# Kernel optimization log

Measured on AMD Instinct MI355X. Metric: run time of the kernel, lower is better.

Reference implementation:

```python
import jax, jax.numpy as jnp
import numpy as np

# Config mirroring MultiHeadAttention1d(in_channels=256, n_heads=8, residual=False,
# kernel_size=1, attention_type=0) applied to 3-D inputs (B, C, N).
B, C, N, H, D = 4, 256, 2048, 8, 256  # per-head dim D = in_channels; OC = H*D = 2048
OC = H * D


def setup_inputs() -> dict:
    key = jax.random.key(0)
    ks = jax.random.split(key, 14)
    s = 1.0 / np.sqrt(C)
    f32 = jnp.float32
    inp = {
        "x": jax.random.normal(ks[0], (B, C, N), f32),
        "y": jax.random.normal(ks[1], (B, C, N), f32),
        # ConvNormActivation1d (kernel_size=1) == pointwise conv + (folded, eval-mode)
        # BatchNorm affine + ReLU. BN folds to per-channel scale g and shift beta.
        "Wq": jax.random.normal(ks[2], (OC, C), f32) * s,
        "bq": jax.random.normal(ks[3], (OC,), f32) * 0.01,
        "gq": jnp.ones((OC,), f32),
        "betaq": jnp.zeros((OC,), f32),
        "Wk": jax.random.normal(ks[4], (OC, C), f32) * s,
        "bk": jax.random.normal(ks[5], (OC,), f32) * 0.01,
        "gk": jnp.ones((OC,), f32),
        "betak": jnp.zeros((OC,), f32),
        "Wv": jax.random.normal(ks[6], (OC, C), f32) * s,
        "bv": jax.random.normal(ks[7], (OC,), f32) * 0.01,
        "gv": jnp.ones((OC,), f32),
        "betav": jnp.zeros((OC,), f32),
    }
    return inp


def _cna(W, b, g, beta, t):
    # 1x1 conv (channel GEMM) + folded-BN affine + ReLU; t: (B, C, N) -> (B, OC, N)
    z = jnp.einsum("oc,bcn->bon", W, t) + b[:, None]
    return jax.nn.relu(g[:, None] * z + beta[:, None])


def _heads(t):
    # (B, OC, N) -> (B, H, N, D); channel split matches torch.split chunks of size D
    return t.reshape(B, H, D, N).transpose(0, 1, 3, 2)


def reference(x, y, Wq, bq, gq, betaq, Wk, bk, gk, betak, Wv, bv, gv, betav):
    q = _heads(_cna(Wq, bq, gq, betaq, x))  # (B,H,N,D)
    k = _heads(_cna(Wk, bk, gk, betak, y))
    v = _heads(_cna(Wv, bv, gv, betav, y))
    energy = jnp.einsum("bhnd,bhmd->bhnm", q, k)  # bmm(Q, K^T)
    attn = jax.nn.softmax(energy, axis=-1)
    out = jnp.einsum("bhnm,bhmd->bhnd", attn, v)  # (B,H,N,D)
    # torch path: view(H,B,k,N,D).permute(1,0,3,2,4) -> (B,H,N,k=1,D);
    # squeeze(dim=2) is a no-op since N != 1.
    return out[:, :, :, None, :]  # (B, H, N, 1, D)
```

## Files before the change

### kernel.cpp

```cpp
#include <hip/hip_runtime.h>
#include <cstdint>
#include <cstddef>

typedef unsigned short u16;
typedef __attribute__((ext_vector_type(4))) float f32x4;
typedef __attribute__((ext_vector_type(16))) float f32x16;
typedef __attribute__((ext_vector_type(8))) _Float16 f16x8;
typedef __attribute__((ext_vector_type(4))) u16   u16x4;
typedef __attribute__((ext_vector_type(8))) u16   u16x8;
typedef __attribute__((ext_vector_type(4))) int   i32x4;

#define DEV static __device__ __forceinline__
#define MFMA16(a,b,c) __builtin_amdgcn_mfma_f32_16x16x32_f16((a),(b),(c),0,0,0)
#define MFMA32(a,b,c) __builtin_amdgcn_mfma_f32_32x32x16_f16((a),(b),(c),0,0,0)

constexpr int Bc = 4, Cc = 256, Nc = 2048, Hc = 8, Dc = 256, OCc = 2048;

constexpr size_t OFF_XT = 0;
constexpr size_t OFF_YT = OFF_XT + (size_t)Bc*Nc*Cc*2;
constexpr size_t OFF_WQ = OFF_YT + (size_t)Bc*Nc*Cc*2;
constexpr size_t OFF_WK = OFF_WQ + (size_t)OCc*Cc*2;
constexpr size_t OFF_WV = OFF_WK + (size_t)OCc*Cc*2;
constexpr size_t OFF_BQ = OFF_WV + (size_t)OCc*Cc*2;
constexpr size_t OFF_BK = OFF_BQ + (size_t)OCc*4;
constexpr size_t OFF_BV = OFF_BK + (size_t)OCc*4;
constexpr size_t OFF_Q  = OFF_BV + (size_t)OCc*4;
constexpr size_t OFF_K  = OFF_Q  + (size_t)Bc*Hc*Nc*Dc*2;
constexpr size_t OFF_V  = OFF_K  + (size_t)Bc*Hc*Nc*Dc*2;

DEV u16 f2h(float x){
  _Float16 h = (_Float16)x;
  return __builtin_bit_cast(u16, h);
}

DEV void load_lds16(const void* g, void* l){
  __builtin_amdgcn_global_load_lds((const __attribute__((address_space(1))) int*)g,
                                   (__attribute__((address_space(3))) int*)l, 16, 0, 0);
}

__global__ __launch_bounds__(256) void transpose_cast(const float* __restrict__ x,
                                                      const float* __restrict__ y,
                                                      u16* __restrict__ XT,
                                                      u16* __restrict__ YT){
  __shared__ u16 tile[64][65];
  int b = blockIdx.z >> 1;
  const float* src = (blockIdx.z & 1) ? y : x;
  u16* dst = (blockIdx.z & 1) ? YT : XT;
  int n0 = blockIdx.x * 64, c0 = blockIdx.y * 64;
  int t = threadIdx.x;
#pragma unroll
  for (int i = 0; i < 16; ++i){
    int slot = i*256 + t;
    int cl = slot >> 6, nl = slot & 63;
    tile[cl][nl] = f2h(src[((size_t)b*Cc + c0 + cl)*Nc + n0 + nl]);
  }
  __syncthreads();
#pragma unroll
  for (int i = 0; i < 8; ++i){
    int slot = i*256 + t;
    int nl = slot >> 5, cl = (slot & 31)*2;
    uint32_t v = (uint32_t)tile[cl][nl] | ((uint32_t)tile[cl+1][nl] << 16);
    *(uint32_t*)(dst + ((size_t)b*Nc + n0 + nl)*Cc + c0 + cl) = v;
  }
}

__global__ __launch_bounds__(256) void prep_w(const float* __restrict__ W,
                                              const float* __restrict__ bsrc,
                                              const float* __restrict__ g,
                                              const float* __restrict__ beta,
                                              u16* __restrict__ Wo,
                                              float* __restrict__ bb){
  int idx = (blockIdx.x*256 + threadIdx.x) * 8;
  int o = idx >> 8, c = idx & 255;
  float gg = g[o];
  f32x4 a0 = *(const f32x4*)(W + idx);
  f32x4 a1 = *(const f32x4*)(W + idx + 4);
  u16x8 r;
#pragma unroll
  for (int i = 0; i < 4; ++i){ r[i] = f2h(a0[i]*gg); r[i+4] = f2h(a1[i]*gg); }
  *(u16x8*)(Wo + idx) = r;
  if (c == 0) bb[o] = gg*bsrc[o] + beta[o];
}

template<int SW>
__global__ __launch_bounds__(256, 2) void proj_gemm(const u16* __restrict__ Xt,
                                                    const u16* __restrict__ Wp,
                                                    const float* __restrict__ bb,
                                                    u16* __restrict__ outp){
  __shared__ __align__(16) char lds[32768];
  int t = threadIdx.x, w = t >> 6, l = t & 63, q = l & 15, g = l >> 4;
  int b = blockIdx.z;
  int n0 = blockIdx.x * 128, o0 = blockIdx.y * 128;
  int fs = ((q >> 1) & 3) << 4;
  int partg = ((l & 3) ^ ((l >> 3) & 3));
  f32x4 acc[4][4] = {};

  for (int it = 0; it < 4; ++it){
    __syncthreads();
#pragma unroll
    for (int j = 0; j < 8; ++j){
      int s = j*4 + w;
      int chunk = s >> 3;
      int off = (s & 7) * 1024;
      int row = (s & 7)*16 + (l >> 2);
      const char* gsrc;
      if (chunk < 2)
        gsrc = (const char*)(Wp + (size_t)(o0 + row)*Cc) + it*128 + chunk*64 + partg*16;
      else
        gsrc = (const char*)(Xt + ((size_t)b*Nc + n0 + row)*Cc) + it*128 + (chunk & 1)*64 + partg*16;
      load_lds16(gsrc, lds + chunk*8192 + off);
    }
    asm volatile("s_waitcnt vmcnt(0)" ::: "memory");
    __syncthreads();
#pragma unroll
    for (int kc = 0; kc < 2; ++kc){
      f16x8 fw[4], fx[4];
#pragma unroll
      for (int i = 0; i < 4; ++i){
        int wrow = (SW ? (w & 1) : (w >> 1))*64 + i*16 + q;
        int xrow = (SW ? (w >> 1) : (w & 1))*64 + i*16 + q;
        fw[i] = *(const f16x8*)(lds + kc*8192 + wrow*64 + ((g*16) ^ fs));
        fx[i] = *(const f16x8*)(lds + 16384 + kc*8192 + xrow*64 + ((g*16) ^ fs));
      }
#pragma unroll
      for (int i = 0; i < 4; ++i)
#pragma unroll
        for (int jj = 0; jj < 4; ++jj){
          if constexpr (!SW) acc[i][jj] = MFMA16(fw[i], fx[jj], acc[i][jj]);
          else               acc[i][jj] = MFMA16(fx[i], fw[jj], acc[i][jj]);
        }
    }
  }

  if constexpr (!SW) {
    f32x4 bias[4];
#pragma unroll
    for (int i = 0; i < 4; ++i) bias[i] = *(const f32x4*)(bb + o0 + (w>>1)*64 + i*16 + 4*g);
#pragma unroll
    for (int i = 0; i < 4; ++i)
#pragma unroll
      for (int jj = 0; jj < 4; ++jj){
        u16x4 pk;
#pragma unroll
        for (int r = 0; r < 4; ++r){
          float z = acc[i][jj][r] + bias[i][r];
          pk[r] = f2h(fmaxf(z, 0.f));
        }
        int o = o0 + (w>>1)*64 + i*16 + 4*g;
        int n = n0 + (w&1)*64 + jj*16 + q;
        int hh = o >> 8, d = o & 255;
        *(u16x4*)(outp + ((size_t)((b*Hc + hh)*Nc + n))*Dc + d) = pk;
      }
  } else {
    float biasv[4];
#pragma unroll
    for (int i = 0; i < 4; ++i) biasv[i] = bb[o0 + (w&1)*64 + i*16 + q];
#pragma unroll
    for (int i = 0; i < 4; ++i)
#pragma unroll
      for (int jj = 0; jj < 4; ++jj){
        u16x4 pk;
#pragma unroll
        for (int r = 0; r < 4; ++r){
          float z = acc[i][jj][r] + biasv[jj];
          pk[r] = f2h(fmaxf(z, 0.f));
        }
        int o = o0 + (w&1)*64 + jj*16 + q;
        int n = n0 + (w>>1)*64 + i*16 + 4*g;
        int hh = o >> 8, d = o & 255;
        *(u16x4*)(outp + ((size_t)((b*Hc + hh)*Dc + d))*Nc + n) = pk;
      }
  }
}

__global__ __launch_bounds__(512, 1) void attn_kernel(const u16* __restrict__ Qp,
                                                      const u16* __restrict__ Kp,
                                                      const u16* __restrict__ Vp,
                                                      float* __restrict__ outp){
  __shared__ __align__(16) char lds[150528];
  const int t = threadIdx.x, w = t >> 6, l = t & 63, lq = l & 31, hi = l >> 5;
  const int wq = w & 3, wm = w >> 2;
  const int h = blockIdx.y, b = blockIdx.z;
  const int q0 = blockIdx.x * 128;
  size_t head = (size_t)(b*Hc + h) * Nc * Dc;
  const u16* Qh = Qp + head;
  const u16* Kh = Kp + head;
  const u16* Vh = Vp + head;

  char* Pex  = lds + 131072;
  float* smax = (float*)(lds + 147456);
  float* ssum = (float*)(lds + 148480);

  f16x8 qf[16];
  {
    const u16* qrow = Qh + (size_t)(q0 + wq*32 + lq) * Dc;
#pragma unroll
    for (int kc = 0; kc < 16; ++kc) qf[kc] = *(const f16x8*)(qrow + kc*16 + hi*8);
  }

  f32x16 acc[4] = {};
  float m_run = -1e30f, l_run = 0.f;
  const int lsw = lq ^ ((lq >> 3) & 3);

#define STAGE_KV(m0_, buf_)                                                        \
  {                                                                                \
    char* Kd = lds + (buf_)*32768;                                                 \
    char* Vd = lds + 65536 + (buf_)*32768;                                         \
    _Pragma("unroll")                                                              \
    for (int j = 0; j < 4; ++j){                                                   \
      int row = w*8 + j*2 + hi;                                                    \
      int r5 = row & 31;                                                           \
      int gs = (l & 31) ^ r5 ^ ((r5 >> 3) & 3);                                    \
      load_lds16(Kh + (size_t)((m0_) + row)*Dc + gs*8, Kd + w*4096 + j*1024);      \
    }                                                                              \
    _Pragma("unroll")                                                              \
    for (int j = 0; j < 4; ++j){                                                   \
      int ri = w*4 + j;                                                            \
      int rd = ri*8 + (l >> 3);                                                    \
      int gs = (l & 7) ^ (rd & 7);                                                 \
      load_lds16(Vh + (size_t)rd*Nc + (m0_) + gs*8, Vd + ri*1024);                 \
    }                                                                              \
  }

  STAGE_KV(0, 0);
  asm volatile("s_waitcnt vmcnt(0)" ::: "memory");
  __syncthreads();

  for (int it = 0; it < 32; ++it){
    const int cur = it & 1;
    char* Kc = lds + cur*32768;
    char* Vc = lds + 65536 + cur*32768;

    if (it < 31) STAGE_KV((it + 1)*64, cur ^ 1);

    f32x16 s = {};
    __builtin_amdgcn_s_setprio(1);
#pragma unroll
    for (int kc = 0; kc < 16; ++kc){
      f16x8 kf = *(const f16x8*)(Kc + (wm*32 + lq)*512 + (((kc*2 + hi) ^ lsw) << 4));
      s = MFMA32(kf, qf[kc], s);
    }
    __builtin_amdgcn_s_setprio(0);

    float tmax = s[0];
#pragma unroll
    for (int r = 1; r < 16; ++r) tmax = fmaxf(tmax, s[r]);
    tmax = fmaxf(tmax, __shfl_xor(tmax, 32));
    if (!hi) smax[(wq*2 + wm)*32 + lq] = tmax;
    __syncthreads();
    float omax = smax[(wq*2 + (1 - wm))*32 + lq];
    float cmax = fmaxf(tmax, omax);

    float meff = m_run, scale = 1.f;
    const bool need = !__all(cmax <= m_run + 8.f);
    if (need){
      meff = fmaxf(m_run, cmax);
      scale = __expf(m_run - meff);
      m_run = meff;
    }

    float p[16];
    float rsum = 0.f;
#pragma unroll
    for (int r = 0; r < 16; ++r){ p[r] = __expf(s[r] - meff); rsum += p[r]; }
    rsum += __shfl_xor(rsum, 32);
    if (!hi) ssum[(wq*2 + wm)*32 + lq] = rsum;

    int pk[8];
#pragma unroll
    for (int j2 = 0; j2 < 8; ++j2)
      pk[j2] = __builtin_bit_cast(int, __builtin_amdgcn_cvt_pkrtz(p[2*j2], p[2*j2+1]));
    int sx[8];
#pragma unroll
    for (int j2 = 0; j2 < 8; ++j2) sx[j2] = __shfl_xor(pk[j2], 32);
    i32x4 f0, f1;
    f0[0] = hi ? sx[2] : pk[0];  f0[1] = hi ? sx[3] : pk[1];
    f0[2] = hi ? pk[2] : sx[0];  f0[3] = hi ? pk[3] : sx[1];
    f1[0] = hi ? sx[6] : pk[4];  f1[1] = hi ? sx[7] : pk[5];
    f1[2] = hi ? pk[6] : sx[4];  f1[3] = hi ? pk[7] : sx[5];
    *(i32x4*)(Pex + w*2048 + l*16)        = f0;
    *(i32x4*)(Pex + w*2048 + 1024 + l*16) = f1;
    __syncthreads();

    float osum = ssum[(wq*2 + (1 - wm))*32 + lq];
    l_run = l_run * scale + rsum + osum;

    if (need){
#pragma unroll
      for (int r = 0; r < 16; ++r){
        float scr = __shfl(scale, (r & 3) + 8*(r >> 2) + 4*hi);
#pragma unroll
        for (int dt = 0; dt < 4; ++dt) acc[dt][r] *= scr;
      }
    }

    i32x4 g0 = *(const i32x4*)(Pex + (w ^ 4)*2048 + l*16);
    i32x4 g1 = *(const i32x4*)(Pex + (w ^ 4)*2048 + 1024 + l*16);
    f16x8 a0 = __builtin_bit_cast(f16x8, wm ? g0 : f0);
    f16x8 a1 = __builtin_bit_cast(f16x8, wm ? g1 : f1);
    f16x8 a2 = __builtin_bit_cast(f16x8, wm ? f0 : g0);
    f16x8 a3 = __builtin_bit_cast(f16x8, wm ? f1 : g1);

    __builtin_amdgcn_s_setprio(1);
#pragma unroll
    for (int h2 = 0; h2 < 2; ++h2)
#pragma unroll
      for (int dt = 0; dt < 4; ++dt)
#pragma unroll
        for (int mcl = 0; mcl < 2; ++mcl){
          f16x8 vf = *(const f16x8*)(Vc + (wm*128 + dt*32 + lq)*128 +
                                     (((h2*4 + mcl*2 + hi)*16) ^ ((l & 7) << 4)));
          f16x8 af = h2 ? (mcl ? a3 : a2) : (mcl ? a1 : a0);
          acc[dt] = MFMA32(af, vf, acc[dt]);
        }
    __builtin_amdgcn_s_setprio(0);

    asm volatile("s_waitcnt vmcnt(0)" ::: "memory");
    __syncthreads();
  }
#undef STAGE_KV

  float inv_own = 1.f / l_run;
#pragma unroll
  for (int r = 0; r < 16; ++r){
    int crow = (r & 3) + 8*(r >> 2) + 4*hi;
    float invr = __shfl(inv_own, crow);
    size_t obase = head + (size_t)(q0 + wq*32 + crow)*Dc + wm*128 + lq;
#pragma unroll
    for (int dt = 0; dt < 4; ++dt)
      outp[obase + dt*32] = acc[dt][r] * invr;
  }
}

extern "C" void kernel_launch(void* const* d_in, const int* in_sizes, int n_in,
                              void* d_out, int out_size, void* d_ws, size_t ws_size,
                              hipStream_t stream){
  const float* x     = (const float*)d_in[0];
  const float* y     = (const float*)d_in[1];
  const float* Wq    = (const float*)d_in[2];
  const float* bq    = (const float*)d_in[3];
  const float* gq    = (const float*)d_in[4];
  const float* betaq = (const float*)d_in[5];
  const float* Wk    = (const float*)d_in[6];
  const float* bk    = (const float*)d_in[7];
  const float* gk    = (const float*)d_in[8];
  const float* betak = (const float*)d_in[9];
  const float* Wv    = (const float*)d_in[10];
  const float* bv    = (const float*)d_in[11];
  const float* gv    = (const float*)d_in[12];
  const float* betav = (const float*)d_in[13];
  char* ws = (char*)d_ws;
  float* outp = (float*)d_out;

  u16* XT = (u16*)(ws + OFF_XT);
  u16* YT = (u16*)(ws + OFF_YT);
  u16* WQb = (u16*)(ws + OFF_WQ);
  u16* WKb = (u16*)(ws + OFF_WK);
  u16* WVb = (u16*)(ws + OFF_WV);
  float* BQ = (float*)(ws + OFF_BQ);
  float* BK = (float*)(ws + OFF_BK);
  float* BV = (float*)(ws + OFF_BV);
  u16* Qw = (u16*)(ws + OFF_Q);
  u16* Kw = (u16*)(ws + OFF_K);
  u16* Vw = (u16*)(ws + OFF_V);

  transpose_cast<<<dim3(Nc/64, Cc/64, Bc*2), 256, 0, stream>>>(x, y, XT, YT);
  prep_w<<<dim3(OCc*Cc/2048), 256, 0, stream>>>(Wq, bq, gq, betaq, WQb, BQ);
  prep_w<<<dim3(OCc*Cc/2048), 256, 0, stream>>>(Wk, bk, gk, betak, WKb, BK);
  prep_w<<<dim3(OCc*Cc/2048), 256, 0, stream>>>(Wv, bv, gv, betav, WVb, BV);

  dim3 pg(Nc/128, OCc/128, Bc);
  proj_gemm<0><<<pg, 256, 0, stream>>>(XT, WQb, BQ, Qw);
  proj_gemm<0><<<pg, 256, 0, stream>>>(YT, WKb, BK, Kw);
  proj_gemm<1><<<pg, 256, 0, stream>>>(YT, WVb, BV, Vw);

  attn_kernel<<<dim3(Nc/128, Hc, Bc), 512, 0, stream>>>(Qw, Kw, Vw, outp);
}
```

Before: 267.7 us.

## Double-buffer projection GEMM LDS loads and merge weight prep launches

The projection GEMM now uses two LDS buffers, prefetching the next K-slice with async global-to-LDS loads while MFMAs run on the current slice. This aims to hide global load latency, which was previously fully exposed before each compute step. The three weight-prep kernels are merged into one launch indexed by blockIdx.y, cutting launch overhead. The doubled LDS (64KB) may reduce occupancy below the launch_bounds target of 2 blocks per CU.

```diff
diff --git a/kernel.cpp b/kernel.cpp
--- a/kernel.cpp
+++ b/kernel.cpp
@@ -64,12 +64,24 @@
   }
 }
 
-__global__ __launch_bounds__(256) void prep_w(const float* __restrict__ W,
-                                              const float* __restrict__ bsrc,
-                                              const float* __restrict__ g,
-                                              const float* __restrict__ beta,
-                                              u16* __restrict__ Wo,
-                                              float* __restrict__ bb){
+__global__ __launch_bounds__(256) void prep_w3(
+    const float* __restrict__ W0, const float* __restrict__ b0,
+    const float* __restrict__ g0, const float* __restrict__ be0,
+    const float* __restrict__ W1, const float* __restrict__ b1,
+    const float* __restrict__ g1, const float* __restrict__ be1,
+    const float* __restrict__ W2, const float* __restrict__ b2,
+    const float* __restrict__ g2, const float* __restrict__ be2,
+    u16* __restrict__ Wo0, float* __restrict__ bb0,
+    u16* __restrict__ Wo1, float* __restrict__ bb1,
+    u16* __restrict__ Wo2, float* __restrict__ bb2){
+  int which = blockIdx.y;
+  const float* W  = (which == 0) ? W0  : (which == 1) ? W1  : W2;
+  const float* bs = (which == 0) ? b0  : (which == 1) ? b1  : b2;
+  const float* g  = (which == 0) ? g0  : (which == 1) ? g1  : g2;
+  const float* be = (which == 0) ? be0 : (which == 1) ? be1 : be2;
+  u16*   Wo = (which == 0) ? Wo0 : (which == 1) ? Wo1 : Wo2;
+  float* bb = (which == 0) ? bb0 : (which == 1) ? bb1 : bb2;
+
   int idx = (blockIdx.x*256 + threadIdx.x) * 8;
   int o = idx >> 8, c = idx & 255;
   float gg = g[o];
@@ -79,7 +91,7 @@
 #pragma unroll
   for (int i = 0; i < 4; ++i){ r[i] = f2h(a0[i]*gg); r[i+4] = f2h(a1[i]*gg); }
   *(u16x8*)(Wo + idx) = r;
-  if (c == 0) bb[o] = gg*bsrc[o] + beta[o];
+  if (c == 0) bb[o] = gg*bs[o] + be[o];
 }
 
 template<int SW>
@@ -87,7 +99,7 @@
                                                     const u16* __restrict__ Wp,
                                                     const float* __restrict__ bb,
                                                     u16* __restrict__ outp){
-  __shared__ __align__(16) char lds[32768];
+  __shared__ __align__(16) char lds[65536];
   int t = threadIdx.x, w = t >> 6, l = t & 63, q = l & 15, g = l >> 4;
   int b = blockIdx.z;
   int n0 = blockIdx.x * 128, o0 = blockIdx.y * 128;
@@ -95,23 +107,32 @@
   int partg = ((l & 3) ^ ((l >> 3) & 3));
   f32x4 acc[4][4] = {};
 
+#define STAGE_P(it_, buf_)                                                            \
+  {                                                                                   \
+    char* base = lds + (buf_)*32768;                                                  \
+    _Pragma("unroll")                                                                 \
+    for (int j = 0; j < 8; ++j){                                                      \
+      int s = j*4 + w;                                                                \
+      int chunk = s >> 3;                                                             \
+      int off = (s & 7) * 1024;                                                       \
+      int row = (s & 7)*16 + (l >> 2);                                                \
+      const char* gsrc;                                                               \
+      if (chunk < 2)                                                                  \
+        gsrc = (const char*)(Wp + (size_t)(o0 + row)*Cc) + (it_)*128 + chunk*64 + partg*16;          \
+      else                                                                            \
+        gsrc = (const char*)(Xt + ((size_t)b*Nc + n0 + row)*Cc) + (it_)*128 + (chunk & 1)*64 + partg*16; \
+      load_lds16(gsrc, base + chunk*8192 + off);                                      \
+    }                                                                                 \
+  }
+
+  STAGE_P(0, 0);
+  asm volatile("s_waitcnt vmcnt(0)" ::: "memory");
+  __syncthreads();
+
   for (int it = 0; it < 4; ++it){
-    __syncthreads();
-#pragma unroll
-    for (int j = 0; j < 8; ++j){
-      int s = j*4 + w;
-      int chunk = s >> 3;
-      int off = (s & 7) * 1024;
-      int row = (s & 7)*16 + (l >> 2);
-      const char* gsrc;
-      if (chunk < 2)
-        gsrc = (const char*)(Wp + (size_t)(o0 + row)*Cc) + it*128 + chunk*64 + partg*16;
-      else
-        gsrc = (const char*)(Xt + ((size_t)b*Nc + n0 + row)*Cc) + it*128 + (chunk & 1)*64 + partg*16;
-      load_lds16(gsrc, lds + chunk*8192 + off);
-    }
-    asm volatile("s_waitcnt vmcnt(0)" ::: "memory");
-    __syncthreads();
+    const int cur = it & 1;
+    char* base = lds + cur*32768;
+    if (it < 3) STAGE_P(it + 1, cur ^ 1);
 #pragma unroll
     for (int kc = 0; kc < 2; ++kc){
       f16x8 fw[4], fx[4];
@@ -119,8 +140,8 @@
       for (int i = 0; i < 4; ++i){
         int wrow = (SW ? (w & 1) : (w >> 1))*64 + i*16 + q;
         int xrow = (SW ? (w >> 1) : (w & 1))*64 + i*16 + q;
-        fw[i] = *(const f16x8*)(lds + kc*8192 + wrow*64 + ((g*16) ^ fs));
-        fx[i] = *(const f16x8*)(lds + 16384 + kc*8192 + xrow*64 + ((g*16) ^ fs));
+        fw[i] = *(const f16x8*)(base + kc*8192 + wrow*64 + ((g*16) ^ fs));
+        fx[i] = *(const f16x8*)(base + 16384 + kc*8192 + xrow*64 + ((g*16) ^ fs));
       }
 #pragma unroll
       for (int i = 0; i < 4; ++i)
@@ -130,7 +151,10 @@
           else               acc[i][jj] = MFMA16(fx[i], fw[jj], acc[i][jj]);
         }
     }
-  }
+    asm volatile("s_waitcnt vmcnt(0)" ::: "memory");
+    __syncthreads();
+  }
+#undef STAGE_P
 
   if constexpr (!SW) {
     f32x4 bias[4];
@@ -365,9 +389,9 @@
   u16* Vw = (u16*)(ws + OFF_V);
 
   transpose_cast<<<dim3(Nc/64, Cc/64, Bc*2), 256, 0, stream>>>(x, y, XT, YT);
-  prep_w<<<dim3(OCc*Cc/2048), 256, 0, stream>>>(Wq, bq, gq, betaq, WQb, BQ);
-  prep_w<<<dim3(OCc*Cc/2048), 256, 0, stream>>>(Wk, bk, gk, betak, WKb, BK);
-  prep_w<<<dim3(OCc*Cc/2048), 256, 0, stream>>>(Wv, bv, gv, betav, WVb, BV);
+  prep_w3<<<dim3(OCc*Cc/2048, 3), 256, 0, stream>>>(
+      Wq, bq, gq, betaq, Wk, bk, gk, betak, Wv, bv, gv, betav,
+      WQb, BQ, WKb, BK, WVb, BV);
 
   dim3 pg(Nc/128, OCc/128, Bc);
   proj_gemm<0><<<pg, 256, 0, stream>>>(XT, WQb, BQ, Qw);
```

New measurement: 274.6 us. 1.03x slower.
